# Kernel optimization log

Measured on AMD Instinct MI355X. Metric: run time of the kernel, lower is better.

The kernel has to match this reference:

```python
import jax, jax.numpy as jnp
import numpy as np

N = 50000      # nodes
E = 800000     # edges (no self-loops; conv adds them)
EMB = 64       # emb_dim
H = 4          # heads
C = EMB // H   # out_channels per head
L = 3          # num_layer
NEG = 0.2      # leaky_relu negative slope
EPS = 1e-5     # batchnorm eps


def setup_inputs() -> dict:
    key = jax.random.key(0)
    ks = jax.random.split(key, 12)
    x_idx = jax.random.randint(ks[0], (N,), 0, 16)
    src = jax.random.randint(ks[1], (E,), 0, N)
    off = jax.random.randint(ks[2], (E,), 1, N)
    dst = (src + off) % N  # guaranteed no self-loops
    edge_index = jnp.stack([src, dst])
    edge_attr_idx = jax.random.randint(ks[3], (E,), 0, 4)
    s = 0.1
    atom_emb = jax.random.normal(ks[4], (16, EMB)) * s
    W = jax.random.normal(ks[5], (L, EMB, H * C)) * s          # lin_src == lin_dst (shared)
    att_src = jax.random.normal(ks[6], (L, H, C)) * s
    att_dst = jax.random.normal(ks[7], (L, H, C)) * s
    att_edge = jax.random.normal(ks[8], (L, H, C)) * s
    bias = jnp.zeros((L, H * C))
    edge_emb = jax.random.normal(ks[9], (L, 4, H * C)) * s     # lin_edge embedding per layer
    bn_gamma = jnp.ones((L, EMB))
    bn_beta = jnp.zeros((L, EMB))
    pred_W = jax.random.normal(ks[10], (2 * EMB, 1)) * s
    pred_b = jnp.zeros((1,))
    return dict(x_idx=x_idx, edge_index=edge_index, edge_attr_idx=edge_attr_idx,
                atom_emb=atom_emb, W=W, att_src=att_src, att_dst=att_dst,
                att_edge=att_edge, bias=bias, edge_emb=edge_emb,
                bn_gamma=bn_gamma, bn_beta=bn_beta, pred_W=pred_W, pred_b=pred_b)


def _gat_forward(x_idx, edge_index, edge_attr_idx, atom_emb, W, att_src, att_dst,
                 att_edge, bias, edge_emb, bn_gamma, bn_beta, pred_W, pred_b):
    src, dst = edge_index[0], edge_index[1]
    loop = jnp.arange(N)
    src2 = jnp.concatenate([src, loop])   # edges + self-loops
    dst2 = jnp.concatenate([dst, loop])
    x = atom_emb[x_idx]                   # [N, EMB]
    for l in range(L):
        # embed edge attrs, self-loop fill = mean of incoming-edge features per node
        ea = edge_emb[l][edge_attr_idx]                                   # [E, H*C]
        cnt = jax.ops.segment_sum(jnp.ones((E,), ea.dtype), dst, N)       # [N]
        ea_mean = jax.ops.segment_sum(ea, dst, N) / jnp.clip(cnt, 1.0)[:, None]
        ea2 = jnp.concatenate([ea, ea_mean]).reshape(-1, H, C)            # [E+N, H, C]
        # shared src/dst projection
        xl = (x @ W[l]).reshape(N, H, C)                                  # [N, H, C]
        a_src = jnp.sum(xl * att_src[l], axis=-1)                         # [N, H]
        a_dst = jnp.sum(xl * att_dst[l], axis=-1)                         # [N, H]
        a_edge = jnp.sum(ea2 * att_edge[l], axis=-1)                      # [E+N, H]
        alpha = a_src[src2] + a_dst[dst2] + a_edge
        alpha = jnp.where(alpha >= 0, alpha, NEG * alpha)                 # leaky_relu
        # segment softmax over incoming edges of each destination node
        m = jax.ops.segment_max(alpha, dst2, N)                           # [N, H]
        ex = jnp.exp(alpha - m[dst2])
        denom = jax.ops.segment_sum(ex, dst2, N)
        alpha = ex / denom[dst2]                                          # [E+N, H]
        # message + scatter-add aggregate
        msg = alpha[:, :, None] * (xl[src2] + ea2)                        # [E+N, H, C]
        out = jax.ops.segment_sum(msg, dst2, N).reshape(N, H * C) + bias[l]
        # BatchNorm1d (training-mode batch stats, biased variance)
        mu = jnp.mean(out, axis=0)
        var = jnp.mean((out - mu) ** 2, axis=0)
        out = (out - mu) * jax.lax.rsqrt(var + EPS) * bn_gamma[l] + bn_beta[l]
        x = jax.nn.relu(out) + x                                          # residual
    pair = jnp.concatenate([x[src], x[dst]], axis=-1)                     # [E, 2*EMB]
    return pair @ pred_W + pred_b                                         # [E, 1]


def reference(x_idx, edge_index, edge_attr_idx, atom_emb, W, att_src, att_dst,
              att_edge, bias, edge_emb, bn_gamma, bn_beta, pred_W, pred_b):
    return _gat_forward(x_idx, edge_index, edge_attr_idx, atom_emb, W, att_src,
                        att_dst, att_edge, bias, edge_emb, bn_gamma, bn_beta,
                        pred_W, pred_b)
```

## Files before the change

### kernel.cpp

```cpp
#include <hip/hip_runtime.h>
#include <hip/hip_bf16.h>

#define NN 50000
#define NE 800000
#define NEG 0.2f
#define BNEPS 1e-5f
#define NB_CVT 61
#define NB_EDGE 3125
#define NB1 200
#define CH1 4000
#define NBKT 250
#define CAPBKT 4096
#define MAXS 512
#define NB_FRONT (NB_CVT + 1 + NB1)
#define NB_MID (NBKT + NN/16)

typedef __hip_bfloat16 bf16;
typedef unsigned short u16;
typedef unsigned int u32;
__device__ __forceinline__ float b2f(bf16 v){ return __bfloat162float(v); }
__device__ __forceinline__ float u2f(u16 u){ return __uint_as_float(((u32)u) << 16); }
__device__ __forceinline__ u16 f2u(float f){ bf16 b = __float2bfloat16(f); return *(u16*)&b; }

struct CvtArgs { const void* src[11]; int off[11]; int cnt[11]; };

__global__ __launch_bounds__(256) void k_front(CvtArgs a, const void* eeraw,
        const void* aeraw, const int* __restrict__ src, const int* __restrict__ dst,
        const int* __restrict__ ety,
        float* __restrict__ cw, float* __restrict__ aet, int* __restrict__ flag,
        int* __restrict__ bcur, u32* __restrict__ bins){
  int t = threadIdx.x, b = blockIdx.x;
  if (b >= NB_CVT + 1){
    __shared__ int cnt[NBKT], start[NBKT], cur[NBKT];
    __shared__ int dcache[CH1];
    int bb = b - (NB_CVT + 1);
    for (int i = t; i < NBKT; i += 256){ cnt[i] = 0; cur[i] = 0; }
    __syncthreads();
    int base = bb*CH1;
    for (int k = t; k < CH1; k += 256){
      int d = dst[base + k];
      dcache[k] = d;
      atomicAdd(&cnt[(u32)d/200u], 1);
    }
    __syncthreads();
    for (int i = t; i < NBKT; i += 256) start[i] = atomicAdd(&bcur[i], cnt[i]);
    __syncthreads();
    for (int k = t; k < CH1; k += 256){
      int e = base + k;
      u32 d = (u32)dcache[k];
      u32 bk = d/200u;
      int pos = start[bk] + atomicAdd(&cur[bk], 1);
      if (pos < CAPBKT)
        bins[bk*CAPBKT + pos] = (u32)src[e] | ((u32)ety[e] << 16) | ((d - bk*200u) << 18);
    }
    return;
  }
  __shared__ int sflag;
  if (t < 64){
    const u16* u = (const u16*)a.src[0];
    int hit = 0;
    for (int i = t; i < 512; i += 64){
      int ex = (u[i] >> 7) & 0xFF;
      if (ex >= 0x8A || (ex != 0 && ex <= 0x60)) hit = 1;
    }
    unsigned long long bl = __ballot(hit);
    if (t == 0) sflag = (bl != 0ULL) ? 1 : 0;
  }
  __syncthreads();
  int f = sflag;
  if (b == 0 && t == 0) *flag = f;
  if (b < NB_CVT){
    int i = b*256 + t;
    #pragma unroll
    for (int s = 0; s < 11; ++s){
      int j = i - a.off[s];
      if (j >= 0 && j < a.cnt[s])
        cw[a.off[s] + j] = f ? ((const float*)a.src[s])[j]
                             : b2f(((const bf16*)a.src[s])[j]);
    }
  } else if (t < 48){
    int l = t >> 4, ty = (t >> 2) & 3, h = t & 3;
    float s = 0.f;
    for (int cc = 0; cc < 16; ++cc){
      int ei = l*256 + ty*64 + h*16 + cc;
      int ai = l*64 + h*16 + cc;
      float ev = f ? ((const float*)eeraw)[ei] : b2f(((const bf16*)eeraw)[ei]);
      float av = f ? ((const float*)aeraw)[ai] : b2f(((const bf16*)aeraw)[ai]);
      s += ev*av;
    }
    aet[t] = s;
  }
}

__global__ __launch_bounds__(256) void k_mid(const int* __restrict__ bcur,
        const u32* __restrict__ bins,
        int* __restrict__ cpack, int* __restrict__ rowst, int* __restrict__ cnt4,
        const int* __restrict__ xidx, const float* __restrict__ aembf,
        const float* __restrict__ Wl, const float* __restrict__ att_s,
        const float* __restrict__ att_d,
        float* __restrict__ x, u16* __restrict__ bxl,
        float* __restrict__ asrc, float* __restrict__ adst){
  __shared__ __align__(16) char smem[17408];
  int t = threadIdx.x, b = blockIdx.x;
  if (b < NBKT){
    int* c4   = (int*)smem;
    int* nst  = c4 + 800;
    int* ncur = nst + 200;
    int* bco  = ncur + 200;
    int* s    = bco + 256;
    for (int i = t; i < 800; i += 256) c4[i] = 0;
    if (t < 200) ncur[t] = 0;
    int v = 0;
    if (t < NBKT){ v = bcur[t]; if (v > CAPBKT) v = CAPBKT; }
    bco[t] = v; s[t] = v;
    __syncthreads();
    for (int o = 1; o < 256; o <<= 1){
      int a2 = s[t]; int add = (t >= o) ? s[t-o] : 0;
      __syncthreads(); s[t] = a2 + add; __syncthreads();
    }
    int gb = s[b] - bco[b];
    int tot = bco[b];
    int total = s[255];
    __syncthreads();
    for (int i = t; i < tot; i += 256){
      u32 e = bins[b*CAPBKT + i];
      atomicAdd(&c4[((e >> 18) & 0xFF)*4 + ((e >> 16) & 3)], 1);
    }
    __syncthreads();
    int deg = 0;
    if (t < 200) deg = c4[t*4] + c4[t*4+1] + c4[t*4+2] + c4[t*4+3];
    s[t] = deg; __syncthreads();
    for (int o = 1; o < 256; o <<= 1){
      int a2 = s[t]; int add = (t >= o) ? s[t-o] : 0;
      __syncthreads(); s[t] = a2 + add; __syncthreads();
    }
    if (t < 200) nst[t] = s[t] - deg;
    __syncthreads();
    if (t < 200){
      int n = b*200 + t;
      rowst[n] = gb + nst[t];
      *(int4*)&cnt4[n*4] = make_int4(c4[t*4], c4[t*4+1], c4[t*4+2], c4[t*4+3]);
    }
    if (b == 0 && t == 0) rowst[NN] = total;
    for (int i = t; i < tot; i += 256){
      u32 e = bins[b*CAPBKT + i];
      int nl = (e >> 18) & 0xFF;
      int pos = nst[nl] + atomicAdd(&ncur[nl], 1);
      cpack[gb + pos] = (int)(e & 0x3FFFF);
    }
    return;
  }
  float* Ws = (float*)smem;
  float* xs = Ws + 4096;
  int bp = b - NBKT;
  for (int i = t; i < 4096; i += 256) Ws[i] = Wl[i];
  int c = t & 63, wv = t >> 6;
  float ats = att_s[c], atd = att_d[c];
  for (int pass = 0; pass < 4; ++pass){
    int n = bp*16 + pass*4 + wv;
    float xv = aembf[xidx[n]*64 + c];
    x[n*64 + c] = xv;
    __syncthreads();
    xs[t] = xv;
    __syncthreads();
    const float* xr = &xs[wv*64];
    float acc = 0.f;
    #pragma unroll
    for (int k = 0; k < 64; ++k) acc += xr[k]*Ws[k*64 + c];
    bxl[n*64 + c] = f2u(acc);
    float vs = acc*ats, vd = acc*atd;
    #pragma unroll
    for (int o = 8; o >= 1; o >>= 1){ vs += __shfl_xor(vs,o,64); vd += __shfl_xor(vd,o,64); }
    if ((c & 15) == 0){ asrc[n*4 + (c>>4)] = vs; adst[n*4 + (c>>4)] = vd; }
  }
}

__global__ __launch_bounds__(256) void k_bnproj(
    const float* __restrict__ opre, const float* __restrict__ bnred,
    const float* __restrict__ gam, const float* __restrict__ bet,
    const float* __restrict__ Wl,
    const float* __restrict__ att_s, const float* __restrict__ att_d,
    float* __restrict__ x, u16* __restrict__ bxl,
    float* __restrict__ asrc, float* __restrict__ adst){
  __shared__ float Ws[4096];
  __shared__ float xs[256];
  int t = threadIdx.x;
  for (int i = t; i < 4096; i += 256) Ws[i] = Wl[i];
  int c = t & 63, wv = t >> 6;
  float mu  = bnred[c] * (1.f/NN);
  float var = bnred[64+c] * (1.f/NN) - mu*mu;
  float rstd = rsqrtf(var + BNEPS);
  float g = gam[c], be = bet[c];
  float ats = att_s[c], atd = att_d[c];
  for (int pass = 0; pass < 4; ++pass){
    int n = blockIdx.x*16 + pass*4 + wv;
    float o = (opre[n*64 + c] - mu)*rstd*g + be;
    float xv = x[n*64 + c] + fmaxf(o, 0.f);
    x[n*64 + c] = xv;
    __syncthreads();
    xs[t] = xv;
    __syncthreads();
    const float* xr = &xs[wv*64];
    float acc = 0.f;
    #pragma unroll
    for (int k = 0; k < 64; ++k) acc += xr[k]*Ws[k*64 + c];
    bxl[n*64 + c] = f2u(acc);
    float vs = acc*ats, vd = acc*atd;
    #pragma unroll
    for (int o2 = 8; o2 >= 1; o2 >>= 1){ vs += __shfl_xor(vs,o2,64); vd += __shfl_xor(vd,o2,64); }
    if ((c & 15) == 0){ asrc[n*4 + (c>>4)] = vs; adst[n*4 + (c>>4)] = vd; }
  }
}

__global__ __launch_bounds__(256) void k_aggr(
    const u16* __restrict__ bxl,
    const float* __restrict__ asrc, const float* __restrict__ adst,
    const int* __restrict__ cnt4, const int* __restrict__ rowst,
    const int* __restrict__ cpack,
    const float* __restrict__ eeg, const float* __restrict__ aetg,
    const float* __restrict__ biasg,
    float* __restrict__ opre, float* __restrict__ bnpart){
  __shared__ float ee[256];
  __shared__ float aetL[16];
  __shared__ float adl[16];
  __shared__ float4 wsh[MAXS];
  __shared__ float redA[256], redB[256];
  __shared__ int rs[5];
  int t = threadIdx.x;
  int n0 = blockIdx.x*4;
  ee[t] = eeg[t];
  if (t < 16){ aetL[t] = aetg[t]; adl[t] = adst[n0*4 + t]; }
  if (t < 5) rs[t] = rowst[n0 + t];
  __syncthreads();
  int jb0 = rs[0], je0 = rs[4], cnt = je0 - jb0;
  int r1 = rs[1], r2 = rs[2], r3 = rs[3];
  int lim = cnt < MAXS ? cnt : MAXS;
  for (int s = t; s < lim; s += 256){
    int j = jb0 + s;
    int pk = cpack[j];
    int sr = pk & 0xFFFF, ty = pk >> 16;
    int dl = (j >= r1) + (j >= r2) + (j >= r3);
    float4 as4 = *(const float4*)&asrc[sr*4];
    float a0 = as4.x + adl[dl*4+0] + aetL[ty*4+0]; a0 = a0>=0.f ? a0 : NEG*a0;
    float a1 = as4.y + adl[dl*4+1] + aetL[ty*4+1]; a1 = a1>=0.f ? a1 : NEG*a1;
    float a2 = as4.z + adl[dl*4+2] + aetL[ty*4+2]; a2 = a2>=0.f ? a2 : NEG*a2;
    float a3 = as4.w + adl[dl*4+3] + aetL[ty*4+3]; a3 = a3>=0.f ? a3 : NEG*a3;
    wsh[s] = make_float4(__expf(a0), __expf(a1), __expf(a2), __expf(a3));
  }
  __syncthreads();
  int wv = t >> 6, c = t & 63, h = c >> 4;
  int n = n0 + wv;
  int jb = rs[wv], je = rs[wv+1];
  int4 c4 = *(const int4*)&cnt4[n*4];
  int deg = c4.x + c4.y + c4.z + c4.w;
  float inv = 1.f / (float)(deg > 0 ? deg : 1);
  float eam = ((float)c4.x*ee[c] + (float)c4.y*ee[64+c]
             + (float)c4.z*ee[128+c] + (float)c4.w*ee[192+c]) * inv;
  float aes = ((float)c4.x*aetL[h] + (float)c4.y*aetL[4+h]
             + (float)c4.z*aetL[8+h] + (float)c4.w*aetL[12+h]) * inv;
  float adn = adl[wv*4 + h];
  float a = asrc[n*4 + h] + adn + aes;
  a = a >= 0.f ? a : NEG*a;
  float wself = __expf(a);
  float den = wself;
  float acc = wself * (u2f(bxl[n*64 + c]) + eam);
  const float* wshf = (const float*)wsh;
  int jlim = jb0 + lim;
  int jeP = je < jlim ? je : jlim;
  int j = jb;
  for (; j + 8 <= jeP; j += 8){
    int so = j - jb0;
    int pk0 = cpack[j],   pk1 = cpack[j+1], pk2 = cpack[j+2], pk3 = cpack[j+3];
    int pk4 = cpack[j+4], pk5 = cpack[j+5], pk6 = cpack[j+6], pk7 = cpack[j+7];
    float w0 = wshf[(so  )*4 + h], w1 = wshf[(so+1)*4 + h];
    float w2 = wshf[(so+2)*4 + h], w3 = wshf[(so+3)*4 + h];
    float w4 = wshf[(so+4)*4 + h], w5 = wshf[(so+5)*4 + h];
    float w6 = wshf[(so+6)*4 + h], w7 = wshf[(so+7)*4 + h];
    int s0=pk0&0xFFFF, s1_=pk1&0xFFFF, s2_=pk2&0xFFFF, s3_=pk3&0xFFFF;
    int s4_=pk4&0xFFFF, s5_=pk5&0xFFFF, s6_=pk6&0xFFFF, s7_=pk7&0xFFFF;
    float x0 = u2f(bxl[s0*64 + c]),  x1 = u2f(bxl[s1_*64 + c]);
    float x2 = u2f(bxl[s2_*64 + c]), x3 = u2f(bxl[s3_*64 + c]);
    float x4 = u2f(bxl[s4_*64 + c]), x5 = u2f(bxl[s5_*64 + c]);
    float x6 = u2f(bxl[s6_*64 + c]), x7 = u2f(bxl[s7_*64 + c]);
    acc += w0*(x0 + ee[(pk0>>16)*64 + c]); den += w0;
    acc += w1*(x1 + ee[(pk1>>16)*64 + c]); den += w1;
    acc += w2*(x2 + ee[(pk2>>16)*64 + c]); den += w2;
    acc += w3*(x3 + ee[(pk3>>16)*64 + c]); den += w3;
    acc += w4*(x4 + ee[(pk4>>16)*64 + c]); den += w4;
    acc += w5*(x5 + ee[(pk5>>16)*64 + c]); den += w5;
    acc += w6*(x6 + ee[(pk6>>16)*64 + c]); den += w6;
    acc += w7*(x7 + ee[(pk7>>16)*64 + c]); den += w7;
  }
  for (; j + 4 <= jeP; j += 4){
    int so = j - jb0;
    int pk0 = cpack[j], pk1 = cpack[j+1], pk2 = cpack[j+2], pk3 = cpack[j+3];
    float w0 = wshf[(so  )*4 + h], w1 = wshf[(so+1)*4 + h];
    float w2 = wshf[(so+2)*4 + h], w3 = wshf[(so+3)*4 + h];
    int s0=pk0&0xFFFF, s1_=pk1&0xFFFF, s2_=pk2&0xFFFF, s3_=pk3&0xFFFF;
    float x0 = u2f(bxl[s0*64 + c]),  x1 = u2f(bxl[s1_*64 + c]);
    float x2 = u2f(bxl[s2_*64 + c]), x3 = u2f(bxl[s3_*64 + c]);
    acc += w0*(x0 + ee[(pk0>>16)*64 + c]); den += w0;
    acc += w1*(x1 + ee[(pk1>>16)*64 + c]); den += w1;
    acc += w2*(x2 + ee[(pk2>>16)*64 + c]); den += w2;
    acc += w3*(x3 + ee[(pk3>>16)*64 + c]); den += w3;
  }
  for (; j < jeP; ++j){
    int pk = cpack[j];
    float wj = wshf[(j - jb0)*4 + h];
    int s_ = pk & 0xFFFF, ty = pk >> 16;
    acc += wj*(u2f(bxl[s_*64 + c]) + ee[ty*64 + c]); den += wj;
  }
  for (; j < je; ++j){
    int pk = cpack[j];
    int s_ = pk & 0xFFFF, ty = pk >> 16;
    float aa = asrc[s_*4 + h] + adn + aetL[ty*4 + h];
    aa = aa >= 0.f ? aa : NEG*aa;
    float wj = __expf(aa);
    acc += wj*(u2f(bxl[s_*64 + c]) + ee[ty*64 + c]); den += wj;
  }
  float out = acc/den + biasg[c];
  opre[n*64 + c] = out;
  redA[t] = out; redB[t] = out*out;
  __syncthreads();
  int part = blockIdx.x & 127;
  if (t < 64){
    atomicAdd(&bnpart[part*128 + t], redA[t]+redA[64+t]+redA[128+t]+redA[192+t]);
  } else if (t < 128){
    int cc = t - 64;
    atomicAdd(&bnpart[part*128 + 64 + cc], redB[cc]+redB[64+cc]+redB[128+cc]+redB[192+cc]);
  }
}

__global__ __launch_bounds__(1024) void k_bnstat(float* __restrict__ bnpart,
                                                 float* __restrict__ bnred){
  __shared__ float red[1024];
  int t = threadIdx.x;
  int c = t & 127, g = t >> 7;
  float s = 0.f;
  for (int p = g; p < 128; p += 8){ s += bnpart[p*128 + c]; bnpart[p*128 + c] = 0.f; }
  red[g*128 + c] = s; __syncthreads();
  if (t < 128){
    float tot = 0.f;
    #pragma unroll
    for (int g2 = 0; g2 < 8; ++g2) tot += red[g2*128 + t];
    bnred[t] = tot;
  }
}

__global__ __launch_bounds__(256) void k_bnpred(
    const float* __restrict__ x, const float* __restrict__ opre,
    const float* __restrict__ bnred, const float* __restrict__ gam,
    const float* __restrict__ bet, const float* __restrict__ pW,
    float* __restrict__ s1, float* __restrict__ s2){
  int t = threadIdx.x, wv = t >> 6, c = t & 63;
  int n = blockIdx.x*4 + wv;
  float mu  = bnred[c] * (1.f/NN);
  float var = bnred[64+c] * (1.f/NN) - mu*mu;
  float o = (opre[n*64 + c] - mu)*rsqrtf(var + BNEPS)*gam[c] + bet[c];
  float xv = x[n*64 + c] + fmaxf(o, 0.f);
  float v1 = xv*pW[c], v2 = xv*pW[64 + c];
  #pragma unroll
  for (int o2 = 32; o2 >= 1; o2 >>= 1){ v1 += __shfl_xor(v1,o2,64); v2 += __shfl_xor(v2,o2,64); }
  if (c == 0){ s1[n] = v1; s2[n] = v2; }
}

__global__ void k_pred_edge(const int* __restrict__ src, const int* __restrict__ dst,
        const float* __restrict__ s1, const float* __restrict__ s2,
        const float* __restrict__ pbf, const int* __restrict__ flag, void* out){
  int e = blockIdx.x*256 + threadIdx.x;
  if (e < NE){
    float v = s1[src[e]] + s2[dst[e]] + pbf[0];
    if (*flag) ((float*)out)[e] = v;
    else       ((bf16*)out)[e] = __float2bfloat16(v);
  }
}

extern "C" void kernel_launch(void* const* d_in, const int* in_sizes, int n_in,
                              void* d_out, int out_size, void* d_ws, size_t ws_size,
                              hipStream_t stream){
  const int*  xidx = (const int*)d_in[0];
  const int*  eidx = (const int*)d_in[1];
  const int*  ety  = (const int*)d_in[2];
  const int* srcp = eidx, *dstp = eidx + NE;

  float* p = (float*)d_ws;
  float* x      = p;            p += NN*64;
  float* opre   = p;            p += NN*64;
  float* asrc   = p;            p += NN*4;
  float* adst   = p;            p += NN*4;
  float* bnred  = p;            p += 128;
  float* s1     = p;            p += NN;
  float* s2     = p;            p += NN;
  float* cw     = p;            p += 15392;
  float* aet    = p;            p += 64;
  float* bnpart = p;            p += 128*128;
  int*   bcur   = (int*)p;
  char*  zend   = (char*)(bcur + 256);
  size_t zbytes = (size_t)(zend - (char*)bnpart);
  u32*   bins   = (u32*)(bcur + 256);
  int*   cpack  = (int*)(bins + NBKT*CAPBKT);
  int*   rowst  = cpack + NE;
  int*   cnt4   = rowst + NN + 4;
  int*   flag   = cnt4 + NN*4;
  u16*   bxl    = (u16*)(flag + 4);

  const int O_AEMB = 0,     N_AEMB = 1024;
  const int O_W    = 1024,  N_W    = 12288;
  const int O_AS   = 13312, N_AS   = 192;
  const int O_AD   = 13504, N_AD   = 192;
  const int O_AE   = 13696, N_AE   = 192;
  const int O_BI   = 13888, N_BI   = 192;
  const int O_EE   = 14080, N_EE   = 768;
  const int O_GA   = 14848, N_GA   = 192;
  const int O_BE   = 15040, N_BE   = 192;
  const int O_PW   = 15232, N_PW   = 128;
  const int O_PB   = 15360, N_PB   = 1;

  CvtArgs ca;
  ca.src[0]=d_in[3];  ca.off[0]=O_AEMB; ca.cnt[0]=N_AEMB;
  ca.src[1]=d_in[4];  ca.off[1]=O_W;    ca.cnt[1]=N_W;
  ca.src[2]=d_in[5];  ca.off[2]=O_AS;   ca.cnt[2]=N_AS;
  ca.src[3]=d_in[6];  ca.off[3]=O_AD;   ca.cnt[3]=N_AD;
  ca.src[4]=d_in[7];  ca.off[4]=O_AE;   ca.cnt[4]=N_AE;
  ca.src[5]=d_in[8];  ca.off[5]=O_BI;   ca.cnt[5]=N_BI;
  ca.src[6]=d_in[9];  ca.off[6]=O_EE;   ca.cnt[6]=N_EE;
  ca.src[7]=d_in[10]; ca.off[7]=O_GA;   ca.cnt[7]=N_GA;
  ca.src[8]=d_in[11]; ca.off[8]=O_BE;   ca.cnt[8]=N_BE;
  ca.src[9]=d_in[12]; ca.off[9]=O_PW;   ca.cnt[9]=N_PW;
  ca.src[10]=d_in[13];ca.off[10]=O_PB;  ca.cnt[10]=N_PB;

  hipMemsetAsync(bnpart, 0, zbytes, stream);
  k_front<<<NB_FRONT, 256, 0, stream>>>(ca, d_in[9], d_in[7], srcp, dstp, ety,
                                        cw, aet, flag, bcur, bins);
  k_mid<<<NB_MID, 256, 0, stream>>>(bcur, bins, cpack, rowst, cnt4,
                                    xidx, cw + O_AEMB, cw + O_W,
                                    cw + O_AS, cw + O_AD, x, bxl, asrc, adst);
  for (int l = 0; l < 3; ++l){
    k_aggr<<<NN/4, 256, 0, stream>>>(bxl, asrc, adst, cnt4, rowst, cpack,
                                     cw + O_EE + l*256, aet + l*16,
                                     cw + O_BI + l*64, opre, bnpart);
    k_bnstat<<<1, 1024, 0, stream>>>(bnpart, bnred);
    if (l < 2)
      k_bnproj<<<NN/16, 256, 0, stream>>>(opre, bnred, cw + O_GA + l*64,
                                          cw + O_BE + l*64, cw + O_W + (l+1)*4096,
                                          cw + O_AS + (l+1)*64, cw + O_AD + (l+1)*64,
                                          x, bxl, asrc, adst);
  }
  k_bnpred<<<NN/4, 256, 0, stream>>>(x, opre, bnred, cw + O_GA + 128,
                                     cw + O_BE + 128, cw + O_PW, s1, s2);
  k_pred_edge<<<NB_EDGE, 256, 0, stream>>>(srcp, dstp, s1, s2, cw + O_PB, flag, d_out);
}
```

Measured before the change: 287.5 us.

## Process eight nodes per aggregation block and cache packed edges in shared memory

The aggregation kernel now handles 8 destination nodes per 256-thread block, with each wave looping over two nodes, and launches half as many blocks. Packed edge entries loaded for the attention-weight precompute are kept in shared memory and reused in the accumulation loop instead of being re-read from global memory. The per-block partial BN sums are also halved, which reduces atomic traffic. The shared edge cache capacity shrinks to 288 while covering twice as many nodes, so more high-degree blocks fall back to the slow recompute path. Each wave also processes its two nodes serially, which reduces parallelism per block.

```diff
diff --git a/kernel.cpp b/kernel.cpp
--- a/kernel.cpp
+++ b/kernel.cpp
@@ -11,7 +11,7 @@
 #define CH1 4000
 #define NBKT 250
 #define CAPBKT 4096
-#define MAXS 512
+#define MAXS 288
 #define NB_FRONT (NB_CVT + 1 + NB1)
 #define NB_MID (NBKT + NN/16)
 
@@ -222,24 +222,26 @@
     float* __restrict__ opre, float* __restrict__ bnpart){
   __shared__ float ee[256];
   __shared__ float aetL[16];
-  __shared__ float adl[16];
+  __shared__ float adl[32];
   __shared__ float4 wsh[MAXS];
+  __shared__ int ents[MAXS];
   __shared__ float redA[256], redB[256];
-  __shared__ int rs[5];
+  __shared__ int rs[9];
   int t = threadIdx.x;
-  int n0 = blockIdx.x*4;
+  int n0 = blockIdx.x*8;
   ee[t] = eeg[t];
-  if (t < 16){ aetL[t] = aetg[t]; adl[t] = adst[n0*4 + t]; }
-  if (t < 5) rs[t] = rowst[n0 + t];
+  if (t < 16) aetL[t] = aetg[t];
+  if (t >= 32 && t < 64) adl[t-32] = adst[n0*4 + (t-32)];
+  if (t >= 64 && t < 73) rs[t-64] = rowst[n0 + (t-64)];
   __syncthreads();
-  int jb0 = rs[0], je0 = rs[4], cnt = je0 - jb0;
-  int r1 = rs[1], r2 = rs[2], r3 = rs[3];
+  int jb0 = rs[0], je0 = rs[8], cnt = je0 - jb0;
   int lim = cnt < MAXS ? cnt : MAXS;
   for (int s = t; s < lim; s += 256){
     int j = jb0 + s;
     int pk = cpack[j];
+    ents[s] = pk;
     int sr = pk & 0xFFFF, ty = pk >> 16;
-    int dl = (j >= r1) + (j >= r2) + (j >= r3);
+    int dl = (j>=rs[1])+(j>=rs[2])+(j>=rs[3])+(j>=rs[4])+(j>=rs[5])+(j>=rs[6])+(j>=rs[7]);
     float4 as4 = *(const float4*)&asrc[sr*4];
     float a0 = as4.x + adl[dl*4+0] + aetL[ty*4+0]; a0 = a0>=0.f ? a0 : NEG*a0;
     float a1 = as4.y + adl[dl*4+1] + aetL[ty*4+1]; a1 = a1>=0.f ? a1 : NEG*a1;
@@ -249,78 +251,80 @@
   }
   __syncthreads();
   int wv = t >> 6, c = t & 63, h = c >> 4;
-  int n = n0 + wv;
-  int jb = rs[wv], je = rs[wv+1];
-  int4 c4 = *(const int4*)&cnt4[n*4];
-  int deg = c4.x + c4.y + c4.z + c4.w;
-  float inv = 1.f / (float)(deg > 0 ? deg : 1);
-  float eam = ((float)c4.x*ee[c] + (float)c4.y*ee[64+c]
-             + (float)c4.z*ee[128+c] + (float)c4.w*ee[192+c]) * inv;
-  float aes = ((float)c4.x*aetL[h] + (float)c4.y*aetL[4+h]
-             + (float)c4.z*aetL[8+h] + (float)c4.w*aetL[12+h]) * inv;
-  float adn = adl[wv*4 + h];
-  float a = asrc[n*4 + h] + adn + aes;
-  a = a >= 0.f ? a : NEG*a;
-  float wself = __expf(a);
-  float den = wself;
-  float acc = wself * (u2f(bxl[n*64 + c]) + eam);
   const float* wshf = (const float*)wsh;
-  int jlim = jb0 + lim;
-  int jeP = je < jlim ? je : jlim;
-  int j = jb;
-  for (; j + 8 <= jeP; j += 8){
-    int so = j - jb0;
-    int pk0 = cpack[j],   pk1 = cpack[j+1], pk2 = cpack[j+2], pk3 = cpack[j+3];
-    int pk4 = cpack[j+4], pk5 = cpack[j+5], pk6 = cpack[j+6], pk7 = cpack[j+7];
-    float w0 = wshf[(so  )*4 + h], w1 = wshf[(so+1)*4 + h];
-    float w2 = wshf[(so+2)*4 + h], w3 = wshf[(so+3)*4 + h];
-    float w4 = wshf[(so+4)*4 + h], w5 = wshf[(so+5)*4 + h];
-    float w6 = wshf[(so+6)*4 + h], w7 = wshf[(so+7)*4 + h];
-    int s0=pk0&0xFFFF, s1_=pk1&0xFFFF, s2_=pk2&0xFFFF, s3_=pk3&0xFFFF;
-    int s4_=pk4&0xFFFF, s5_=pk5&0xFFFF, s6_=pk6&0xFFFF, s7_=pk7&0xFFFF;
-    float x0 = u2f(bxl[s0*64 + c]),  x1 = u2f(bxl[s1_*64 + c]);
-    float x2 = u2f(bxl[s2_*64 + c]), x3 = u2f(bxl[s3_*64 + c]);
-    float x4 = u2f(bxl[s4_*64 + c]), x5 = u2f(bxl[s5_*64 + c]);
-    float x6 = u2f(bxl[s6_*64 + c]), x7 = u2f(bxl[s7_*64 + c]);
-    acc += w0*(x0 + ee[(pk0>>16)*64 + c]); den += w0;
-    acc += w1*(x1 + ee[(pk1>>16)*64 + c]); den += w1;
-    acc += w2*(x2 + ee[(pk2>>16)*64 + c]); den += w2;
-    acc += w3*(x3 + ee[(pk3>>16)*64 + c]); den += w3;
-    acc += w4*(x4 + ee[(pk4>>16)*64 + c]); den += w4;
-    acc += w5*(x5 + ee[(pk5>>16)*64 + c]); den += w5;
-    acc += w6*(x6 + ee[(pk6>>16)*64 + c]); den += w6;
-    acc += w7*(x7 + ee[(pk7>>16)*64 + c]); den += w7;
-  }
-  for (; j + 4 <= jeP; j += 4){
-    int so = j - jb0;
-    int pk0 = cpack[j], pk1 = cpack[j+1], pk2 = cpack[j+2], pk3 = cpack[j+3];
-    float w0 = wshf[(so  )*4 + h], w1 = wshf[(so+1)*4 + h];
-    float w2 = wshf[(so+2)*4 + h], w3 = wshf[(so+3)*4 + h];
-    int s0=pk0&0xFFFF, s1_=pk1&0xFFFF, s2_=pk2&0xFFFF, s3_=pk3&0xFFFF;
-    float x0 = u2f(bxl[s0*64 + c]),  x1 = u2f(bxl[s1_*64 + c]);
-    float x2 = u2f(bxl[s2_*64 + c]), x3 = u2f(bxl[s3_*64 + c]);
-    acc += w0*(x0 + ee[(pk0>>16)*64 + c]); den += w0;
-    acc += w1*(x1 + ee[(pk1>>16)*64 + c]); den += w1;
-    acc += w2*(x2 + ee[(pk2>>16)*64 + c]); den += w2;
-    acc += w3*(x3 + ee[(pk3>>16)*64 + c]); den += w3;
-  }
-  for (; j < jeP; ++j){
-    int pk = cpack[j];
-    float wj = wshf[(j - jb0)*4 + h];
-    int s_ = pk & 0xFFFF, ty = pk >> 16;
-    acc += wj*(u2f(bxl[s_*64 + c]) + ee[ty*64 + c]); den += wj;
-  }
-  for (; j < je; ++j){
-    int pk = cpack[j];
-    int s_ = pk & 0xFFFF, ty = pk >> 16;
-    float aa = asrc[s_*4 + h] + adn + aetL[ty*4 + h];
-    aa = aa >= 0.f ? aa : NEG*aa;
-    float wj = __expf(aa);
-    acc += wj*(u2f(bxl[s_*64 + c]) + ee[ty*64 + c]); den += wj;
-  }
-  float out = acc/den + biasg[c];
-  opre[n*64 + c] = out;
-  redA[t] = out; redB[t] = out*out;
+  float sA = 0.f, sB = 0.f;
+  #pragma unroll
+  for (int half = 0; half < 2; ++half){
+    int node = wv + half*4;
+    int n = n0 + node;
+    int jb = rs[node], je = rs[node+1];
+    int4 c4 = *(const int4*)&cnt4[n*4];
+    int deg = c4.x + c4.y + c4.z + c4.w;
+    float inv = 1.f / (float)(deg > 0 ? deg : 1);
+    float eam = ((float)c4.x*ee[c] + (float)c4.y*ee[64+c]
+               + (float)c4.z*ee[128+c] + (float)c4.w*ee[192+c]) * inv;
+    float aes = ((float)c4.x*aetL[h] + (float)c4.y*aetL[4+h]
+               + (float)c4.z*aetL[8+h] + (float)c4.w*aetL[12+h]) * inv;
+    float adn = adl[node*4 + h];
+    float a = asrc[n*4 + h] + adn + aes;
+    a = a >= 0.f ? a : NEG*a;
+    float wself = __expf(a);
+    float den = wself;
+    float acc = wself * (u2f(bxl[n*64 + c]) + eam);
+    int jlim = jb0 + lim;
+    int jeP = je < jlim ? je : jlim;
+    int j = jb;
+    for (; j + 8 <= jeP; j += 8){
+      int so = j - jb0;
+      int pk0 = ents[so],   pk1 = ents[so+1], pk2 = ents[so+2], pk3 = ents[so+3];
+      int pk4 = ents[so+4], pk5 = ents[so+5], pk6 = ents[so+6], pk7 = ents[so+7];
+      float w0 = wshf[(so  )*4 + h], w1 = wshf[(so+1)*4 + h];
+      float w2 = wshf[(so+2)*4 + h], w3 = wshf[(so+3)*4 + h];
+      float w4 = wshf[(so+4)*4 + h], w5 = wshf[(so+5)*4 + h];
+      float w6 = wshf[(so+6)*4 + h], w7 = wshf[(so+7)*4 + h];
+      float x0 = u2f(bxl[(pk0&0xFFFF)*64 + c]), x1 = u2f(bxl[(pk1&0xFFFF)*64 + c]);
+      float x2 = u2f(bxl[(pk2&0xFFFF)*64 + c]), x3 = u2f(bxl[(pk3&0xFFFF)*64 + c]);
+      float x4 = u2f(bxl[(pk4&0xFFFF)*64 + c]), x5 = u2f(bxl[(pk5&0xFFFF)*64 + c]);
+      float x6 = u2f(bxl[(pk6&0xFFFF)*64 + c]), x7 = u2f(bxl[(pk7&0xFFFF)*64 + c]);
+      acc += w0*(x0 + ee[(pk0>>16)*64 + c]); den += w0;
+      acc += w1*(x1 + ee[(pk1>>16)*64 + c]); den += w1;
+      acc += w2*(x2 + ee[(pk2>>16)*64 + c]); den += w2;
+      acc += w3*(x3 + ee[(pk3>>16)*64 + c]); den += w3;
+      acc += w4*(x4 + ee[(pk4>>16)*64 + c]); den += w4;
+      acc += w5*(x5 + ee[(pk5>>16)*64 + c]); den += w5;
+      acc += w6*(x6 + ee[(pk6>>16)*64 + c]); den += w6;
+      acc += w7*(x7 + ee[(pk7>>16)*64 + c]); den += w7;
+    }
+    for (; j + 4 <= jeP; j += 4){
+      int so = j - jb0;
+      int pk0 = ents[so], pk1 = ents[so+1], pk2 = ents[so+2], pk3 = ents[so+3];
+      float w0 = wshf[(so  )*4 + h], w1 = wshf[(so+1)*4 + h];
+      float w2 = wshf[(so+2)*4 + h], w3 = wshf[(so+3)*4 + h];
+      float x0 = u2f(bxl[(pk0&0xFFFF)*64 + c]), x1 = u2f(bxl[(pk1&0xFFFF)*64 + c]);
+      float x2 = u2f(bxl[(pk2&0xFFFF)*64 + c]), x3 = u2f(bxl[(pk3&0xFFFF)*64 + c]);
+      acc += w0*(x0 + ee[(pk0>>16)*64 + c]); den += w0;
+      acc += w1*(x1 + ee[(pk1>>16)*64 + c]); den += w1;
+      acc += w2*(x2 + ee[(pk2>>16)*64 + c]); den += w2;
+      acc += w3*(x3 + ee[(pk3>>16)*64 + c]); den += w3;
+    }
+    for (; j < jeP; ++j){
+      int pk = ents[j - jb0];
+      float wj = wshf[(j - jb0)*4 + h];
+      acc += wj*(u2f(bxl[(pk&0xFFFF)*64 + c]) + ee[(pk>>16)*64 + c]); den += wj;
+    }
+    for (; j < je; ++j){
+      int pk = cpack[j];
+      int s_ = pk & 0xFFFF, ty = pk >> 16;
+      float aa = asrc[s_*4 + h] + adn + aetL[ty*4 + h];
+      aa = aa >= 0.f ? aa : NEG*aa;
+      float wj = __expf(aa);
+      acc += wj*(u2f(bxl[s_*64 + c]) + ee[ty*64 + c]); den += wj;
+    }
+    float out = acc/den + biasg[c];
+    opre[n*64 + c] = out;
+    sA += out; sB += out*out;
+  }
+  redA[t] = sA; redB[t] = sB;
   __syncthreads();
   int part = blockIdx.x & 127;
   if (t < 64){
@@ -436,7 +440,7 @@
                                     xidx, cw + O_AEMB, cw + O_W,
                                     cw + O_AS, cw + O_AD, x, bxl, asrc, adst);
   for (int l = 0; l < 3; ++l){
-    k_aggr<<<NN/4, 256, 0, stream>>>(bxl, asrc, adst, cnt4, rowst, cpack,
+    k_aggr<<<NN/8, 256, 0, stream>>>(bxl, asrc, adst, cnt4, rowst, cpack,
                                      cw + O_EE + l*256, aet + l*16,
                                      cw + O_BI + l*64, opre, bnpart);
     k_bnstat<<<1, 1024, 0, stream>>>(bnpart, bnred);
```

New measurement: 251.1 us. 1.15x faster.
